# Kernel tuning notes

Hardware: AMD Instinct MI355X
Metric: run time of the kernel (lower is better)

Reference implementation:

```python
import jax, jax.numpy as jnp
import numpy as np

B, T, D_IN = 64, 1024, 12
H = 256          # hidden_dim
N_CLASSES = 17


def _lstm_dir(x, w_ih, w_hh, b_ih, b_hh, reverse):
    """Single-direction LSTM. x: [B,T,D]; w_ih: [4H,D]; w_hh: [4H,H]. Returns [B,T,H].
    Gate order follows PyTorch: i, f, g, o."""
    # Precompute input projection for all timesteps (big GEMM, compute-friendly)
    x_proj = jnp.einsum('btd,gd->btg', x, w_ih) + (b_ih + b_hh)  # [B,T,4H]
    x_proj = jnp.swapaxes(x_proj, 0, 1)  # [T,B,4H]
    h0 = jnp.zeros((x.shape[0], H), x.dtype)
    c0 = jnp.zeros((x.shape[0], H), x.dtype)

    def step(carry, xt):
        h, c = carry
        gates = xt + h @ w_hh.T  # [B,4H]
        i, f, g, o = jnp.split(gates, 4, axis=-1)
        c = jax.nn.sigmoid(f) * c + jax.nn.sigmoid(i) * jnp.tanh(g)
        h = jax.nn.sigmoid(o) * jnp.tanh(c)
        return (h, c), h

    _, hs = jax.lax.scan(step, (h0, c0), x_proj, reverse=reverse)  # hs: [T,B,H]
    return jnp.swapaxes(hs, 0, 1)  # [B,T,H]


def _bilstm_layer(x, w_ih, w_hh, b_ih, b_hh):
    """w_*: stacked [2, ...] for (forward, backward) directions."""
    fwd = _lstm_dir(x, w_ih[0], w_hh[0], b_ih[0], b_hh[0], reverse=False)
    bwd = _lstm_dir(x, w_ih[1], w_hh[1], b_ih[1], b_hh[1], reverse=True)
    return jnp.concatenate([fwd, bwd], axis=-1)  # [B,T,2H]


def setup_inputs() -> dict:
    key = jax.random.key(0)
    ks = jax.random.split(key, 11)
    s = 1.0 / np.sqrt(H)  # PyTorch LSTM init scale
    x = jax.random.normal(ks[0], (B, T, D_IN), dtype=jnp.float32)
    # Layer 0: input dim D_IN; Layer 1: input dim 2H (bidirectional outputs)
    w_ih0 = jax.random.uniform(ks[1], (2, 4 * H, D_IN), minval=-s, maxval=s)
    w_hh0 = jax.random.uniform(ks[2], (2, 4 * H, H), minval=-s, maxval=s)
    b_ih0 = jax.random.uniform(ks[3], (2, 4 * H), minval=-s, maxval=s)
    b_hh0 = jax.random.uniform(ks[4], (2, 4 * H), minval=-s, maxval=s)
    w_ih1 = jax.random.uniform(ks[5], (2, 4 * H, 2 * H), minval=-s, maxval=s)
    w_hh1 = jax.random.uniform(ks[6], (2, 4 * H, H), minval=-s, maxval=s)
    b_ih1 = jax.random.uniform(ks[7], (2, 4 * H), minval=-s, maxval=s)
    b_hh1 = jax.random.uniform(ks[8], (2, 4 * H), minval=-s, maxval=s)
    fc_w = jax.random.uniform(ks[9], (N_CLASSES, 2 * H), minval=-s, maxval=s)
    fc_b = jax.random.uniform(ks[10], (N_CLASSES,), minval=-s, maxval=s)
    return {"x": x, "w_ih0": w_ih0, "w_hh0": w_hh0, "b_ih0": b_ih0, "b_hh0": b_hh0,
            "w_ih1": w_ih1, "w_hh1": w_hh1, "b_ih1": b_ih1, "b_hh1": b_hh1,
            "fc_w": fc_w, "fc_b": fc_b}


def reference(x, w_ih0, w_hh0, b_ih0, b_hh0, w_ih1, w_hh1, b_ih1, b_hh1, fc_w, fc_b):
    # Eval mode: dropout layers are identity.
    h = _bilstm_layer(x, w_ih0, w_hh0, b_ih0, b_hh0)   # [B,T,2H]
    h = _bilstm_layer(h, w_ih1, w_hh1, b_ih1, b_hh1)   # [B,T,2H]
    pooled = h.mean(axis=1)                             # [B,2H]
    return pooled @ fc_w.T + fc_b                       # [B,n_classes]
```

## Files before the change

kernel.cpp:

```cpp
#include <hip/hip_runtime.h>

#define NB 64
#define NT 1024
#define DIN 12
#define NH 256
#define NG 1024
#define NCLS 17
#define TCL 128
#define NCHUNK 8
#define XPS ((size_t)2 * NB * TCL * NG)

typedef _Float16 f16;
typedef __attribute__((ext_vector_type(2))) _Float16 half2_t;
typedef __attribute__((ext_vector_type(8))) _Float16 f16x8;
typedef __attribute__((ext_vector_type(4))) float f32x4;
typedef unsigned int uint;
typedef unsigned short ushort;

__device__ __forceinline__ float sigm(float v) { return 1.0f / (1.0f + __expf(-v)); }
__device__ __forceinline__ float tanh_(float v) {
    v = fminf(fmaxf(v, -15.0f), 15.0f);
    float e = __expf(2.0f * v);
    return (e - 1.0f) / (e + 1.0f);
}
__device__ __forceinline__ float dot2(uint w, uint h, float c) {
    return __builtin_amdgcn_fdot2(__builtin_bit_cast(half2_t, w),
                                  __builtin_bit_cast(half2_t, h), c, false);
}
__device__ __forceinline__ uint pack16(float a, float b) {
    union { f16 h[2]; uint u; } cv; cv.h[0] = (f16)a; cv.h[1] = (f16)b; return cv.u;
}
__device__ __forceinline__ uint pkrtz(float a, float b) {
    return __builtin_bit_cast(uint, __builtin_amdgcn_cvt_pkrtz(a, b));
}
__device__ __forceinline__ ushort hbits(f16 v) {
    union { f16 h; ushort u; } cv; cv.h = v; return cv.u;
}

__global__ void k_prep(const float* __restrict__ w_hh0, const float* __restrict__ w_hh1,
                       const float* __restrict__ w_ih0, const float* __restrict__ w_ih1,
                       const float* __restrict__ b_ih1, const float* __restrict__ b_hh1,
                       uint* __restrict__ Wkv, uint* __restrict__ Wka,
                       uint* __restrict__ Wkl, uint* __restrict__ wih0p,
                       f16* __restrict__ wih1h, float* __restrict__ bsum1) {
    int i = blockIdx.x * 256 + threadIdx.x;
    if (i < 4 * 4 * 256 * 40) {
        int kp = i % 40; int r = i / 40;
        int t = r & 255, q = (r >> 8) & 3, ld = r >> 10;
        const float* row = (ld < 2 ? w_hh0 : w_hh1) + (size_t)(ld & 1) * NG * NH
                         + (size_t)(q * 256 + t) * NH;
        Wkv[i] = pack16(row[2 * kp], row[2 * kp + 1]);
    }
    if (i < 4 * 4 * 256 * 60) {
        int kp = 40 + (i % 60); int r = i / 60;
        int t = r & 255, q = (r >> 8) & 3, ld = r >> 10;
        const float* row = (ld < 2 ? w_hh0 : w_hh1) + (size_t)(ld & 1) * NG * NH
                         + (size_t)(q * 256 + t) * NH;
        Wka[i] = pack16(row[2 * kp], row[2 * kp + 1]);
    }
    if (i < 4 * 4 * 7 * 256 * 4) {
        int j = i & 3; int u = i >> 2;
        int t = u & 255; int v = u >> 8;
        int g = v % 7; int w2 = v / 7;
        int q = w2 & 3, ld = w2 >> 2;
        int kp = 100 + 4 * g + j;
        const float* row = (ld < 2 ? w_hh0 : w_hh1) + (size_t)(ld & 1) * NG * NH
                         + (size_t)(q * 256 + t) * NH;
        Wkl[i] = pack16(row[2 * kp], row[2 * kp + 1]);
    }
    if (i < 2 * 4 * 6 * 256) {
        int t = i & 255; int r = i >> 8;
        int dp = r % 6, q = (r / 6) & 3, dd = r / 24;
        const float* row = w_ih0 + ((size_t)dd * NG + q * 256 + t) * DIN;
        wih0p[i] = pack16(row[2 * dp], row[2 * dp + 1]);
    }
    if (i < 2 * NG * 2 * NH) wih1h[i] = (f16)w_ih1[i];
    if (i < 2 * NG) bsum1[i] = b_ih1[i] + b_hh1[i];
}

template <int LAYER>
__device__ void rec_seq(char* smem, int rb, int chunk, int nsteps,
                        const uint* __restrict__ Wkv, const uint* __restrict__ Wka,
                        const uint* __restrict__ Wkl, const uint* __restrict__ wih0p,
                        const float* __restrict__ b_ih0, const float* __restrict__ b_hh0,
                        const float* __restrict__ x, const float* __restrict__ xp1,
                        f16* __restrict__ out0h,
                        float* __restrict__ hst, float* __restrict__ cst,
                        float* __restrict__ hsm) {
    uint4* wlds4 = (uint4*)smem;
    ushort* hs16 = (ushort*)(smem + 114688);
    uint* wihl = (uint*)(smem + 115712);

    const int tid = threadIdx.x;
    const int dir = rb >> 6;
    const int b = rb & 63;
    const int ld = LAYER * 2 + dir;

    for (int n = tid; n < 7168; n += 256) wlds4[n] = ((const uint4*)Wkl)[ld * 7168 + n];
    if (LAYER == 0)
        for (int n = tid; n < 6144; n += 256) wihl[n] = wih0p[dir * 6144 + n];

    uint4 wrv[4][10];
    #pragma unroll
    for (int q = 0; q < 4; ++q) {
        const uint* src = Wkv + (size_t)((ld * 4 + q) * 256 + tid) * 40;
        #pragma unroll
        for (int m = 0; m < 10; ++m) wrv[q][m] = *(const uint4*)(src + m * 4);
    }

    uint aw[240];
    #pragma unroll
    for (int q = 0; q < 4; ++q) {
        const uint* src = Wka + (size_t)((ld * 4 + q) * 256 + tid) * 60;
        #pragma unroll
        for (int m = 0; m < 15; ++m) {
            uint4 v = *(const uint4*)(src + m * 4);
            asm volatile("v_accvgpr_write_b32 %0, %1" : "=a"(aw[(q * 15 + m) * 4 + 0]) : "v"(v.x));
            asm volatile("v_accvgpr_write_b32 %0, %1" : "=a"(aw[(q * 15 + m) * 4 + 1]) : "v"(v.y));
            asm volatile("v_accvgpr_write_b32 %0, %1" : "=a"(aw[(q * 15 + m) * 4 + 2]) : "v"(v.z));
            asm volatile("v_accvgpr_write_b32 %0, %1" : "=a"(aw[(q * 15 + m) * 4 + 3]) : "v"(v.w));
        }
    }

    float bias[4] = {0.f, 0.f, 0.f, 0.f};
    if (LAYER == 0) {
        #pragma unroll
        for (int q = 0; q < 4; ++q)
            bias[q] = b_ih0[dir * NG + q * 256 + tid] + b_hh0[dir * NG + q * 256 + tid];
    }

    const int sidx = (ld * NB + b) * NH + tid;
    float cv, hv, hsv = 0.f;
    if (chunk == 0) { cv = 0.f; hv = 0.f; }
    else {
        cv = cst[sidx]; hv = hst[sidx];
        if (LAYER == 1) hsv = hsm[(dir * NB + b) * NH + tid];
    }
    hs16[tid] = hbits((f16)hv);
    __syncthreads();

    #pragma unroll 1
    for (int it = 0; it < nsteps; ++it) {
        const int par = it & 1;
        const uint4* Hh = (const uint4*)(hs16 + par * 256);

        float ah[4] = {0, 0, 0, 0};

        float xv[12]; float4 xq4;
        if (LAYER == 0) {
            const int t = dir ? (NT - 1 - it) : it;
            const float4* xp = (const float4*)(x + ((size_t)b * NT + t) * DIN);
            float4 A = xp[0], B4 = xp[1], C4 = xp[2];
            xv[0] = A.x;  xv[1] = A.y;  xv[2] = A.z;  xv[3] = A.w;
            xv[4] = B4.x; xv[5] = B4.y; xv[6] = B4.z; xv[7] = B4.w;
            xv[8] = C4.x; xv[9] = C4.y; xv[10] = C4.z; xv[11] = C4.w;
        } else {
            xq4 = *(const float4*)(xp1 + (((size_t)dir * NB + b) * TCL + it) * NG + tid * 4);
        }

        #pragma unroll
        for (int g8 = 0; g8 < 10; ++g8) {
            uint4 Hhv = Hh[g8];
            #pragma unroll
            for (int q = 0; q < 4; ++q) {
                uint4 w = wrv[q][g8];
                ah[q] = dot2(w.x, Hhv.x, ah[q]);
                ah[q] = dot2(w.y, Hhv.y, ah[q]);
                ah[q] = dot2(w.z, Hhv.z, ah[q]);
                ah[q] = dot2(w.w, Hhv.w, ah[q]);
            }
        }
        #pragma unroll
        for (int m = 0; m < 15; ++m) {
            const int g8 = 10 + m;
            uint4 Hhv = Hh[g8];
            #pragma unroll
            for (int q = 0; q < 4; ++q) {
                uint w0, w1, w2, w3;
                asm volatile("v_accvgpr_read_b32 %0, %1" : "=v"(w0) : "a"(aw[(q * 15 + m) * 4 + 0]));
                asm volatile("v_accvgpr_read_b32 %0, %1" : "=v"(w1) : "a"(aw[(q * 15 + m) * 4 + 1]));
                asm volatile("v_accvgpr_read_b32 %0, %1" : "=v"(w2) : "a"(aw[(q * 15 + m) * 4 + 2]));
                asm volatile("v_accvgpr_read_b32 %0, %1" : "=v"(w3) : "a"(aw[(q * 15 + m) * 4 + 3]));
                ah[q] = dot2(w0, Hhv.x, ah[q]);
                ah[q] = dot2(w1, Hhv.y, ah[q]);
                ah[q] = dot2(w2, Hhv.z, ah[q]);
                ah[q] = dot2(w3, Hhv.w, ah[q]);
            }
        }
        #pragma unroll
        for (int g = 0; g < 7; ++g) {
            const int g8 = 25 + g;
            uint4 Hhv = Hh[g8];
            #pragma unroll
            for (int q = 0; q < 4; ++q) {
                uint4 w = wlds4[(q * 7 + g) * 256 + tid];
                ah[q] = dot2(w.x, Hhv.x, ah[q]);
                ah[q] = dot2(w.y, Hhv.y, ah[q]);
                ah[q] = dot2(w.z, Hhv.z, ah[q]);
                ah[q] = dot2(w.w, Hhv.w, ah[q]);
            }
        }

        float z[4];
        #pragma unroll
        for (int q = 0; q < 4; ++q) z[q] = ah[q];
        if (LAYER == 0) {
            uint xph[6];
            #pragma unroll
            for (int d = 0; d < 6; ++d) xph[d] = pkrtz(xv[2 * d], xv[2 * d + 1]);
            #pragma unroll
            for (int q = 0; q < 4; ++q) {
                float a = bias[q];
                #pragma unroll
                for (int d = 0; d < 6; ++d)
                    a = dot2(wihl[(q * 6 + d) * 256 + tid], xph[d], a);
                z[q] += a;
            }
        } else {
            z[0] += xq4.x; z[1] += xq4.y; z[2] += xq4.z; z[3] += xq4.w;
        }
        cv = sigm(z[1]) * cv + sigm(z[0]) * tanh_(z[2]);
        hv = sigm(z[3]) * tanh_(cv);
        if (LAYER == 1) hsv += hv;

        f16 hi = (f16)hv;
        hs16[(par ^ 1) * 256 + tid] = hbits(hi);
        if (LAYER == 0) {
            const int t = dir ? (NT - 1 - it) : it;
            out0h[((size_t)b * NT + t) * 512 + dir * 256 + tid] = hi;
        }
        __syncthreads();
    }

    cst[sidx] = cv; hst[sidx] = hv;
    if (LAYER == 1) hsm[(dir * NB + b) * NH + tid] = hsv;
}

__device__ void proj_role(int pb, int c,
                          const f16* __restrict__ out0h, const f16* __restrict__ wih1h,
                          const float* __restrict__ bsum1, float* __restrict__ xp1) {
    const int tid = threadIdx.x;
    const int w = tid >> 6, l = tid & 63;
    const int lane16 = l & 15, quad = l >> 4;

    #pragma unroll 1
    for (int mi = 0; mi < 2; ++mi) {
        const int mtg = pb * 8 + w * 2 + mi;
        const int dirt = mtg >> 9;
        const int mtl = mtg & 511;

        const int ra = mtl * 16 + lane16;
        const int ab = ra >> 7, tla = ra & 127;
        const int ta = dirt ? (NT - 1 - c * TCL - tla) : (c * TCL + tla);
        const f16* Arow = out0h + ((size_t)ab * NT + ta) * 512 + quad * 8;

        uint4 afr[16];
        #pragma unroll
        for (int kt = 0; kt < 16; ++kt) afr[kt] = *(const uint4*)(Arow + kt * 32);

        int ob[4], otl[4];
        #pragma unroll
        for (int reg = 0; reg < 4; ++reg) {
            int rr = mtl * 16 + quad * 4 + reg;
            ob[reg] = rr >> 7; otl[reg] = rr & 127;
        }

        const f16* Bbase = wih1h + (size_t)dirt * NG * 512 + quad * 8;

        #pragma unroll 1
        for (int nt = 0; nt < 64; ++nt) {
            const int col = nt * 16 + lane16;
            const f16* Brow = Bbase + (size_t)col * 512;
            float bias = bsum1[dirt * NG + col];

            f32x4 acc = {0.f, 0.f, 0.f, 0.f};
            #pragma unroll
            for (int kt = 0; kt < 16; ++kt) {
                uint4 bv = *(const uint4*)(Brow + kt * 32);
                acc = __builtin_amdgcn_mfma_f32_16x16x32_f16(
                    __builtin_bit_cast(f16x8, afr[kt]),
                    __builtin_bit_cast(f16x8, bv), acc, 0, 0, 0);
            }
            const int ucol = col & 255, qcol = col >> 8;
            #pragma unroll
            for (int reg = 0; reg < 4; ++reg) {
                xp1[((size_t)(dirt * NB + ob[reg]) * TCL + otl[reg]) * NG
                    + ucol * 4 + qcol] = acc[reg] + bias;
            }
        }
    }
}

__global__ __launch_bounds__(256, 1) void k_rec0(
    const uint* __restrict__ Wkv, const uint* __restrict__ Wka,
    const uint* __restrict__ Wkl, const uint* __restrict__ wih0p,
    const float* __restrict__ b_ih0, const float* __restrict__ b_hh0,
    const float* __restrict__ x, f16* __restrict__ out0h,
    float* __restrict__ hst, float* __restrict__ cst) {
    extern __shared__ __align__(16) char smem[];
    rec_seq<0>(smem, blockIdx.x, 0, NT, Wkv, Wka, Wkl, wih0p, b_ih0, b_hh0,
               x, nullptr, out0h, hst, cst, nullptr);
}

__global__ __launch_bounds__(256, 1) void k_pipe(
    int j,
    const uint* __restrict__ Wkv, const uint* __restrict__ Wka,
    const uint* __restrict__ Wkl,
    const f16* __restrict__ out0h, const f16* __restrict__ wih1h,
    const float* __restrict__ bsum1, float* __restrict__ xp1,
    float* __restrict__ hst, float* __restrict__ cst, float* __restrict__ hsm) {
    extern __shared__ __align__(16) char smem[];
    const int bid = blockIdx.x;
    if (bid < 128) {
        const int cc = j - 1;
        if (cc >= 0 && cc < NCHUNK)
            rec_seq<1>(smem, bid, cc, TCL, Wkv, Wka, Wkl, nullptr, nullptr, nullptr,
                       nullptr, xp1 + (size_t)(cc & 1) * XPS, nullptr, hst, cst, hsm);
    } else {
        const int cp = j;
        if (cp < NCHUNK)
            proj_role(bid - 128, cp, out0h, wih1h, bsum1,
                      xp1 + (size_t)(cp & 1) * XPS);
    }
}

__global__ void k_fc(const float* __restrict__ hsm, const float* __restrict__ fc_w,
                     const float* __restrict__ fc_b, float* __restrict__ out) {
    const int b = blockIdx.x;
    const int n = threadIdx.x;
    if (n >= NCLS) return;
    float acc = fc_b[n];
    const float inv = 1.0f / (float)NT;
    for (int k = 0; k < 2 * NH; ++k) {
        float pv = hsm[((k >> 8) * NB + b) * NH + (k & 255)];
        acc += (pv * inv) * fc_w[n * 2 * NH + k];
    }
    out[b * NCLS + n] = acc;
}

extern "C" void kernel_launch(void* const* d_in, const int* in_sizes, int n_in,
                              void* d_out, int out_size, void* d_ws, size_t ws_size,
                              hipStream_t stream) {
    const float* x     = (const float*)d_in[0];
    const float* w_ih0 = (const float*)d_in[1];
    const float* w_hh0 = (const float*)d_in[2];
    const float* b_ih0 = (const float*)d_in[3];
    const float* b_hh0 = (const float*)d_in[4];
    const float* w_ih1 = (const float*)d_in[5];
    const float* w_hh1 = (const float*)d_in[6];
    const float* b_ih1 = (const float*)d_in[7];
    const float* b_hh1 = (const float*)d_in[8];
    const float* fc_w  = (const float*)d_in[9];
    const float* fc_b  = (const float*)d_in[10];
    float* out = (float*)d_out;

    char* ws = (char*)d_ws;
    uint* Wkv   = (uint*)ws;
    uint* Wka   = Wkv + 163840;
    uint* Wkl   = Wka + 245760;
    uint* wih0p = Wkl + 114688;
    f16* wih1h  = (f16*)(wih0p + 12288);
    float* bsum1 = (float*)(wih1h + 1048576);
    float* hst  = bsum1 + 2048;
    float* cst  = hst + 65536;
    float* hsm  = cst + 65536;
    float* xp1  = hsm + 32768;
    f16* out0h  = (f16*)(xp1 + 2 * XPS);

    k_prep<<<dim3(4096), dim3(256), 0, stream>>>(
        w_hh0, w_hh1, w_ih0, w_ih1, b_ih1, b_hh1,
        Wkv, Wka, Wkl, wih0p, wih1h, bsum1);

    k_rec0<<<dim3(128), dim3(256), 140288, stream>>>(
        Wkv, Wka, Wkl, wih0p, b_ih0, b_hh0, x, out0h, hst, cst);

    for (int j = 0; j <= NCHUNK; ++j) {
        k_pipe<<<dim3(256), dim3(256), 115712, stream>>>(
            j, Wkv, Wka, Wkl, out0h, wih1h, bsum1, xp1, hst, cst, hsm);
    }

    k_fc<<<dim3(64), dim3(32), 0, stream>>>(hsm, fc_w, fc_b, out);
}
```

Measured before the change: 4.978 ms.

## Split LSTM recurrence K-dimension across two thread halves per block

Each recurrent block now runs 512 threads. Each hidden unit's 256-wide dot product is split into two K halves, one per thread group, and the partial gate sums are combined through shared memory with an extra barrier per step. Weight packing is reorganised so each half keeps a smaller set of weights in VGPRs/AGPRs and the remainder in LDS. The projection role now handles one M tile per wave, since twice as many waves are available. This shortens the serial per-step dot-product chain at the cost of an additional __syncthreads and LDS exchange on every timestep.

```diff
diff --git a/kernel.cpp b/kernel.cpp
--- a/kernel.cpp
+++ b/kernel.cpp
@@ -44,35 +44,37 @@
                        uint* __restrict__ Wkl, uint* __restrict__ wih0p,
                        f16* __restrict__ wih1h, float* __restrict__ bsum1) {
     int i = blockIdx.x * 256 + threadIdx.x;
-    if (i < 4 * 4 * 256 * 40) {
-        int kp = i % 40; int r = i / 40;
-        int t = r & 255, q = (r >> 8) & 3, ld = r >> 10;
+    if (i < 131072) {
+        int kpi = i & 15; int r = i >> 4;
+        int u = r & 255, pp = (r >> 8) & 1, q = (r >> 9) & 3, ld = r >> 11;
         const float* row = (ld < 2 ? w_hh0 : w_hh1) + (size_t)(ld & 1) * NG * NH
-                         + (size_t)(q * 256 + t) * NH;
+                         + (size_t)(q * 256 + u) * NH;
+        int kp = 64 * pp + kpi;
         Wkv[i] = pack16(row[2 * kp], row[2 * kp + 1]);
     }
-    if (i < 4 * 4 * 256 * 60) {
-        int kp = 40 + (i % 60); int r = i / 60;
-        int t = r & 255, q = (r >> 8) & 3, ld = r >> 10;
+    if (i < 262144) {
+        int kpi = i & 31; int r = i >> 5;
+        int u = r & 255, pp = (r >> 8) & 1, q = (r >> 9) & 3, ld = r >> 11;
         const float* row = (ld < 2 ? w_hh0 : w_hh1) + (size_t)(ld & 1) * NG * NH
-                         + (size_t)(q * 256 + t) * NH;
+                         + (size_t)(q * 256 + u) * NH;
+        int kp = 64 * pp + 16 + kpi;
         Wka[i] = pack16(row[2 * kp], row[2 * kp + 1]);
     }
-    if (i < 4 * 4 * 7 * 256 * 4) {
-        int j = i & 3; int u = i >> 2;
-        int t = u & 255; int v = u >> 8;
-        int g = v % 7; int w2 = v / 7;
-        int q = w2 & 3, ld = w2 >> 2;
-        int kp = 100 + 4 * g + j;
+    if (i < 131072) {
+        int j = i & 3; int r4 = i >> 2;
+        int u = r4 & 255, pp = (r4 >> 8) & 1, g4 = (r4 >> 9) & 3;
+        int q = (r4 >> 11) & 3, ld = r4 >> 13;
         const float* row = (ld < 2 ? w_hh0 : w_hh1) + (size_t)(ld & 1) * NG * NH
-                         + (size_t)(q * 256 + t) * NH;
+                         + (size_t)(q * 256 + u) * NH;
+        int kp = 64 * pp + 48 + 4 * g4 + j;
         Wkl[i] = pack16(row[2 * kp], row[2 * kp + 1]);
     }
-    if (i < 2 * 4 * 6 * 256) {
-        int t = i & 255; int r = i >> 8;
-        int dp = r % 6, q = (r / 6) & 3, dd = r / 24;
-        const float* row = w_ih0 + ((size_t)dd * NG + q * 256 + t) * DIN;
-        wih0p[i] = pack16(row[2 * dp], row[2 * dp + 1]);
+    if (i < 12288) {
+        int dp = i % 3; int r = i / 3;
+        int u = r & 255, pp = (r >> 8) & 1, q = (r >> 9) & 3, dd = r >> 11;
+        const float* row = w_ih0 + ((size_t)dd * NG + q * 256 + u) * DIN;
+        int d0 = 6 * pp + 2 * dp;
+        wih0p[i] = pack16(row[d0], row[d0 + 1]);
     }
     if (i < 2 * NG * 2 * NH) wih1h[i] = (f16)w_ih1[i];
     if (i < 2 * NG) bsum1[i] = b_ih1[i] + b_hh1[i];
@@ -81,159 +83,166 @@
 template <int LAYER>
 __device__ void rec_seq(char* smem, int rb, int chunk, int nsteps,
                         const uint* __restrict__ Wkv, const uint* __restrict__ Wka,
-                        const uint* __restrict__ Wkl, const uint* __restrict__ wih0p,
+                        const uint4* __restrict__ Wkl, const uint* __restrict__ wih0p,
                         const float* __restrict__ b_ih0, const float* __restrict__ b_hh0,
                         const float* __restrict__ x, const float* __restrict__ xp1,
                         f16* __restrict__ out0h,
                         float* __restrict__ hst, float* __restrict__ cst,
                         float* __restrict__ hsm) {
     uint4* wlds4 = (uint4*)smem;
-    ushort* hs16 = (ushort*)(smem + 114688);
-    uint* wihl = (uint*)(smem + 115712);
-
+    float* zx = (float*)(smem + 131072);
+    ushort* hs16 = (ushort*)(smem + 135168);
     const int tid = threadIdx.x;
-    const int dir = rb >> 6;
-    const int b = rb & 63;
+    const int u = tid & 255, p = tid >> 8;
+    const int dir = rb >> 6, b = rb & 63;
     const int ld = LAYER * 2 + dir;
 
-    for (int n = tid; n < 7168; n += 256) wlds4[n] = ((const uint4*)Wkl)[ld * 7168 + n];
-    if (LAYER == 0)
-        for (int n = tid; n < 6144; n += 256) wihl[n] = wih0p[dir * 6144 + n];
-
-    uint4 wrv[4][10];
+    for (int n = tid; n < 8192; n += 512) wlds4[n] = Wkl[ld * 8192 + n];
+
+    uint4 wrv[4][4];
     #pragma unroll
     for (int q = 0; q < 4; ++q) {
-        const uint* src = Wkv + (size_t)((ld * 4 + q) * 256 + tid) * 40;
-        #pragma unroll
-        for (int m = 0; m < 10; ++m) wrv[q][m] = *(const uint4*)(src + m * 4);
-    }
-
-    uint aw[240];
+        const uint* src = Wkv + (size_t)((((ld * 4 + q) * 2 + p) * 256) + u) * 16;
+        #pragma unroll
+        for (int gi = 0; gi < 4; ++gi) wrv[q][gi] = *(const uint4*)(src + gi * 4);
+    }
+    uint aw[128];
     #pragma unroll
     for (int q = 0; q < 4; ++q) {
-        const uint* src = Wka + (size_t)((ld * 4 + q) * 256 + tid) * 60;
-        #pragma unroll
-        for (int m = 0; m < 15; ++m) {
-            uint4 v = *(const uint4*)(src + m * 4);
-            asm volatile("v_accvgpr_write_b32 %0, %1" : "=a"(aw[(q * 15 + m) * 4 + 0]) : "v"(v.x));
-            asm volatile("v_accvgpr_write_b32 %0, %1" : "=a"(aw[(q * 15 + m) * 4 + 1]) : "v"(v.y));
-            asm volatile("v_accvgpr_write_b32 %0, %1" : "=a"(aw[(q * 15 + m) * 4 + 2]) : "v"(v.z));
-            asm volatile("v_accvgpr_write_b32 %0, %1" : "=a"(aw[(q * 15 + m) * 4 + 3]) : "v"(v.w));
-        }
-    }
-
+        const uint* src = Wka + (size_t)((((ld * 4 + q) * 2 + p) * 256) + u) * 32;
+        #pragma unroll
+        for (int ga = 0; ga < 8; ++ga) {
+            uint4 v = *(const uint4*)(src + ga * 4);
+            asm volatile("v_accvgpr_write_b32 %0, %1" : "=a"(aw[(q * 8 + ga) * 4 + 0]) : "v"(v.x));
+            asm volatile("v_accvgpr_write_b32 %0, %1" : "=a"(aw[(q * 8 + ga) * 4 + 1]) : "v"(v.y));
+            asm volatile("v_accvgpr_write_b32 %0, %1" : "=a"(aw[(q * 8 + ga) * 4 + 2]) : "v"(v.z));
+            asm volatile("v_accvgpr_write_b32 %0, %1" : "=a"(aw[(q * 8 + ga) * 4 + 3]) : "v"(v.w));
+        }
+    }
+
+    uint wihr[12];
+    if (LAYER == 0) {
+        #pragma unroll
+        for (int q = 0; q < 4; ++q) {
+            const uint* src = wih0p + (size_t)((((dir * 4 + q) * 2 + p) * 256) + u) * 3;
+            wihr[q * 3 + 0] = src[0]; wihr[q * 3 + 1] = src[1]; wihr[q * 3 + 2] = src[2];
+        }
+    }
     float bias[4] = {0.f, 0.f, 0.f, 0.f};
-    if (LAYER == 0) {
+    if (LAYER == 0 && p == 0) {
         #pragma unroll
         for (int q = 0; q < 4; ++q)
-            bias[q] = b_ih0[dir * NG + q * 256 + tid] + b_hh0[dir * NG + q * 256 + tid];
-    }
-
-    const int sidx = (ld * NB + b) * NH + tid;
-    float cv, hv, hsv = 0.f;
-    if (chunk == 0) { cv = 0.f; hv = 0.f; }
-    else {
-        cv = cst[sidx]; hv = hst[sidx];
-        if (LAYER == 1) hsv = hsm[(dir * NB + b) * NH + tid];
-    }
-    hs16[tid] = hbits((f16)hv);
+            bias[q] = b_ih0[dir * NG + q * 256 + u] + b_hh0[dir * NG + q * 256 + u];
+    }
+
+    const int sidx = (ld * NB + b) * NH + u;
+    float cv = 0.f, hv = 0.f, hsv = 0.f;
+    if (p == 0) {
+        if (chunk != 0) {
+            cv = cst[sidx]; hv = hst[sidx];
+            if (LAYER == 1) hsv = hsm[(dir * NB + b) * NH + u];
+        }
+        hs16[u] = hbits((f16)hv);
+    }
     __syncthreads();
 
     #pragma unroll 1
     for (int it = 0; it < nsteps; ++it) {
-        const int par = it & 1;
-        const uint4* Hh = (const uint4*)(hs16 + par * 256);
-
-        float ah[4] = {0, 0, 0, 0};
-
-        float xv[12]; float4 xq4;
-        if (LAYER == 0) {
+        const uint4* Hh = ((const uint4*)hs16) + 16 * p;
+
+        float4 xq4 = {0.f, 0.f, 0.f, 0.f};
+        float xvp[6];
+        if (LAYER == 1) {
+            if (p == 0)
+                xq4 = *(const float4*)(xp1 + (((size_t)dir * NB + b) * TCL + it) * NG + u * 4);
+        } else {
             const int t = dir ? (NT - 1 - it) : it;
             const float4* xp = (const float4*)(x + ((size_t)b * NT + t) * DIN);
             float4 A = xp[0], B4 = xp[1], C4 = xp[2];
-            xv[0] = A.x;  xv[1] = A.y;  xv[2] = A.z;  xv[3] = A.w;
-            xv[4] = B4.x; xv[5] = B4.y; xv[6] = B4.z; xv[7] = B4.w;
-            xv[8] = C4.x; xv[9] = C4.y; xv[10] = C4.z; xv[11] = C4.w;
-        } else {
-            xq4 = *(const float4*)(xp1 + (((size_t)dir * NB + b) * TCL + it) * NG + tid * 4);
-        }
-
-        #pragma unroll
-        for (int g8 = 0; g8 < 10; ++g8) {
-            uint4 Hhv = Hh[g8];
+            if (p == 0) { xvp[0]=A.x; xvp[1]=A.y; xvp[2]=A.z; xvp[3]=A.w; xvp[4]=B4.x; xvp[5]=B4.y; }
+            else        { xvp[0]=B4.z; xvp[1]=B4.w; xvp[2]=C4.x; xvp[3]=C4.y; xvp[4]=C4.z; xvp[5]=C4.w; }
+        }
+
+        float ah[4] = {0.f, 0.f, 0.f, 0.f};
+
+        #pragma unroll
+        for (int gi = 0; gi < 4; ++gi) {
+            uint4 H = Hh[gi];
             #pragma unroll
             for (int q = 0; q < 4; ++q) {
-                uint4 w = wrv[q][g8];
-                ah[q] = dot2(w.x, Hhv.x, ah[q]);
-                ah[q] = dot2(w.y, Hhv.y, ah[q]);
-                ah[q] = dot2(w.z, Hhv.z, ah[q]);
-                ah[q] = dot2(w.w, Hhv.w, ah[q]);
-            }
-        }
-        #pragma unroll
-        for (int m = 0; m < 15; ++m) {
-            const int g8 = 10 + m;
-            uint4 Hhv = Hh[g8];
+                uint4 w = wrv[q][gi];
+                ah[q] = dot2(w.x, H.x, ah[q]);
+                ah[q] = dot2(w.y, H.y, ah[q]);
+                ah[q] = dot2(w.z, H.z, ah[q]);
+                ah[q] = dot2(w.w, H.w, ah[q]);
+            }
+        }
+        #pragma unroll
+        for (int ga = 0; ga < 8; ++ga) {
+            uint4 H = Hh[4 + ga];
             #pragma unroll
             for (int q = 0; q < 4; ++q) {
                 uint w0, w1, w2, w3;
-                asm volatile("v_accvgpr_read_b32 %0, %1" : "=v"(w0) : "a"(aw[(q * 15 + m) * 4 + 0]));
-                asm volatile("v_accvgpr_read_b32 %0, %1" : "=v"(w1) : "a"(aw[(q * 15 + m) * 4 + 1]));
-                asm volatile("v_accvgpr_read_b32 %0, %1" : "=v"(w2) : "a"(aw[(q * 15 + m) * 4 + 2]));
-                asm volatile("v_accvgpr_read_b32 %0, %1" : "=v"(w3) : "a"(aw[(q * 15 + m) * 4 + 3]));
-                ah[q] = dot2(w0, Hhv.x, ah[q]);
-                ah[q] = dot2(w1, Hhv.y, ah[q]);
-                ah[q] = dot2(w2, Hhv.z, ah[q]);
-                ah[q] = dot2(w3, Hhv.w, ah[q]);
-            }
-        }
-        #pragma unroll
-        for (int g = 0; g < 7; ++g) {
-            const int g8 = 25 + g;
-            uint4 Hhv = Hh[g8];
+                asm volatile("v_accvgpr_read_b32 %0, %1" : "=v"(w0) : "a"(aw[(q * 8 + ga) * 4 + 0]));
+                asm volatile("v_accvgpr_read_b32 %0, %1" : "=v"(w1) : "a"(aw[(q * 8 + ga) * 4 + 1]));
+                asm volatile("v_accvgpr_read_b32 %0, %1" : "=v"(w2) : "a"(aw[(q * 8 + ga) * 4 + 2]));
+                asm volatile("v_accvgpr_read_b32 %0, %1" : "=v"(w3) : "a"(aw[(q * 8 + ga) * 4 + 3]));
+                ah[q] = dot2(w0, H.x, ah[q]);
+                ah[q] = dot2(w1, H.y, ah[q]);
+                ah[q] = dot2(w2, H.z, ah[q]);
+                ah[q] = dot2(w3, H.w, ah[q]);
+            }
+        }
+        #pragma unroll
+        for (int g4 = 0; g4 < 4; ++g4) {
+            uint4 H = Hh[12 + g4];
             #pragma unroll
             for (int q = 0; q < 4; ++q) {
-                uint4 w = wlds4[(q * 7 + g) * 256 + tid];
-                ah[q] = dot2(w.x, Hhv.x, ah[q]);
-                ah[q] = dot2(w.y, Hhv.y, ah[q]);
-                ah[q] = dot2(w.z, Hhv.z, ah[q]);
-                ah[q] = dot2(w.w, Hhv.w, ah[q]);
-            }
-        }
-
-        float z[4];
-        #pragma unroll
-        for (int q = 0; q < 4; ++q) z[q] = ah[q];
+                uint4 w = wlds4[((q * 4 + g4) * 2 + p) * 256 + u];
+                ah[q] = dot2(w.x, H.x, ah[q]);
+                ah[q] = dot2(w.y, H.y, ah[q]);
+                ah[q] = dot2(w.z, H.z, ah[q]);
+                ah[q] = dot2(w.w, H.w, ah[q]);
+            }
+        }
         if (LAYER == 0) {
-            uint xph[6];
-            #pragma unroll
-            for (int d = 0; d < 6; ++d) xph[d] = pkrtz(xv[2 * d], xv[2 * d + 1]);
+            uint xph[3];
+            #pragma unroll
+            for (int dp = 0; dp < 3; ++dp) xph[dp] = pkrtz(xvp[2 * dp], xvp[2 * dp + 1]);
             #pragma unroll
             for (int q = 0; q < 4; ++q) {
-                float a = bias[q];
-                #pragma unroll
-                for (int d = 0; d < 6; ++d)
-                    a = dot2(wihl[(q * 6 + d) * 256 + tid], xph[d], a);
-                z[q] += a;
-            }
-        } else {
-            z[0] += xq4.x; z[1] += xq4.y; z[2] += xq4.z; z[3] += xq4.w;
-        }
-        cv = sigm(z[1]) * cv + sigm(z[0]) * tanh_(z[2]);
-        hv = sigm(z[3]) * tanh_(cv);
-        if (LAYER == 1) hsv += hv;
-
-        f16 hi = (f16)hv;
-        hs16[(par ^ 1) * 256 + tid] = hbits(hi);
-        if (LAYER == 0) {
-            const int t = dir ? (NT - 1 - it) : it;
-            out0h[((size_t)b * NT + t) * 512 + dir * 256 + tid] = hi;
-        }
+                ah[q] = dot2(wihr[q * 3 + 0], xph[0], ah[q]);
+                ah[q] = dot2(wihr[q * 3 + 1], xph[1], ah[q]);
+                ah[q] = dot2(wihr[q * 3 + 2], xph[2], ah[q]);
+            }
+        }
+
+        if (p == 1) *(float4*)(zx + u * 4) = make_float4(ah[0], ah[1], ah[2], ah[3]);
         __syncthreads();
-    }
-
-    cst[sidx] = cv; hst[sidx] = hv;
-    if (LAYER == 1) hsm[(dir * NB + b) * NH + tid] = hsv;
+
+        if (p == 0) {
+            float4 zo = *(const float4*)(zx + u * 4);
+            float z0 = ah[0] + zo.x + bias[0] + xq4.x;
+            float z1 = ah[1] + zo.y + bias[1] + xq4.y;
+            float z2 = ah[2] + zo.z + bias[2] + xq4.z;
+            float z3 = ah[3] + zo.w + bias[3] + xq4.w;
+            cv = sigm(z1) * cv + sigm(z0) * tanh_(z2);
+            hv = sigm(z3) * tanh_(cv);
+            if (LAYER == 1) hsv += hv;
+            f16 hi = (f16)hv;
+            hs16[u] = hbits(hi);
+            if (LAYER == 0) {
+                const int t = dir ? (NT - 1 - it) : it;
+                out0h[((size_t)b * NT + t) * 512 + dir * 256 + u] = hi;
+            }
+        }
+        __syncthreads();
+    }
+
+    if (p == 0) {
+        cst[sidx] = cv; hst[sidx] = hv;
+        if (LAYER == 1) hsm[(dir * NB + b) * NH + u] = hsv;
+    }
 }
 
 __device__ void proj_role(int pb, int c,
@@ -242,58 +251,54 @@
     const int tid = threadIdx.x;
     const int w = tid >> 6, l = tid & 63;
     const int lane16 = l & 15, quad = l >> 4;
+    const int mtg = pb * 8 + w;
+    const int dirt = mtg >> 9;
+    const int mtl = mtg & 511;
+
+    const int ra = mtl * 16 + lane16;
+    const int ab = ra >> 7, tla = ra & 127;
+    const int ta = dirt ? (NT - 1 - c * TCL - tla) : (c * TCL + tla);
+    const f16* Arow = out0h + ((size_t)ab * NT + ta) * 512 + quad * 8;
+
+    uint4 afr[16];
+    #pragma unroll
+    for (int kt = 0; kt < 16; ++kt) afr[kt] = *(const uint4*)(Arow + kt * 32);
+
+    int ob[4], otl[4];
+    #pragma unroll
+    for (int reg = 0; reg < 4; ++reg) {
+        int rr = mtl * 16 + quad * 4 + reg;
+        ob[reg] = rr >> 7; otl[reg] = rr & 127;
+    }
+
+    const f16* Bbase = wih1h + (size_t)dirt * NG * 512 + quad * 8;
 
     #pragma unroll 1
-    for (int mi = 0; mi < 2; ++mi) {
-        const int mtg = pb * 8 + w * 2 + mi;
-        const int dirt = mtg >> 9;
-        const int mtl = mtg & 511;
-
-        const int ra = mtl * 16 + lane16;
-        const int ab = ra >> 7, tla = ra & 127;
-        const int ta = dirt ? (NT - 1 - c * TCL - tla) : (c * TCL + tla);
-        const f16* Arow = out0h + ((size_t)ab * NT + ta) * 512 + quad * 8;
-
-        uint4 afr[16];
-        #pragma unroll
-        for (int kt = 0; kt < 16; ++kt) afr[kt] = *(const uint4*)(Arow + kt * 32);
-
-        int ob[4], otl[4];
+    for (int nt = 0; nt < 64; ++nt) {
+        const int col = nt * 16 + lane16;
+        const f16* Brow = Bbase + (size_t)col * 512;
+        float bias = bsum1[dirt * NG + col];
+
+        f32x4 acc = {0.f, 0.f, 0.f, 0.f};
+        #pragma unroll
+        for (int kt = 0; kt < 16; ++kt) {
+            uint4 bv = *(const uint4*)(Brow + kt * 32);
+            acc = __builtin_amdgcn_mfma_f32_16x16x32_f16(
+                __builtin_bit_cast(f16x8, afr[kt]),
+                __builtin_bit_cast(f16x8, bv), acc, 0, 0, 0);
+        }
+        const int ucol = col & 255, qcol = col >> 8;
         #pragma unroll
         for (int reg = 0; reg < 4; ++reg) {
-            int rr = mtl * 16 + quad * 4 + reg;
-            ob[reg] = rr >> 7; otl[reg] = rr & 127;
-        }
-
-        const f16* Bbase = wih1h + (size_t)dirt * NG * 512 + quad * 8;
-
-        #pragma unroll 1
-        for (int nt = 0; nt < 64; ++nt) {
-            const int col = nt * 16 + lane16;
-            const f16* Brow = Bbase + (size_t)col * 512;
-            float bias = bsum1[dirt * NG + col];
-
-            f32x4 acc = {0.f, 0.f, 0.f, 0.f};
-            #pragma unroll
-            for (int kt = 0; kt < 16; ++kt) {
-                uint4 bv = *(const uint4*)(Brow + kt * 32);
-                acc = __builtin_amdgcn_mfma_f32_16x16x32_f16(
-                    __builtin_bit_cast(f16x8, afr[kt]),
-                    __builtin_bit_cast(f16x8, bv), acc, 0, 0, 0);
-            }
-            const int ucol = col & 255, qcol = col >> 8;
-            #pragma unroll
-            for (int reg = 0; reg < 4; ++reg) {
-                xp1[((size_t)(dirt * NB + ob[reg]) * TCL + otl[reg]) * NG
-                    + ucol * 4 + qcol] = acc[reg] + bias;
-            }
-        }
-    }
-}
-
-__global__ __launch_bounds__(256, 1) void k_rec0(
+            xp1[((size_t)(dirt * NB + ob[reg]) * TCL + otl[reg]) * NG
+                + ucol * 4 + qcol] = acc[reg] + bias;
+        }
+    }
+}
+
+__global__ __launch_bounds__(512) void k_rec0(
     const uint* __restrict__ Wkv, const uint* __restrict__ Wka,
-    const uint* __restrict__ Wkl, const uint* __restrict__ wih0p,
+    const uint4* __restrict__ Wkl, const uint* __restrict__ wih0p,
     const float* __restrict__ b_ih0, const float* __restrict__ b_hh0,
     const float* __restrict__ x, f16* __restrict__ out0h,
     float* __restrict__ hst, float* __restrict__ cst) {
@@ -302,10 +307,10 @@
                x, nullptr, out0h, hst, cst, nullptr);
 }
 
-__global__ __launch_bounds__(256, 1) void k_pipe(
+__global__ __launch_bounds__(512) void k_pipe(
     int j,
     const uint* __restrict__ Wkv, const uint* __restrict__ Wka,
-    const uint* __restrict__ Wkl,
+    const uint4* __restrict__ Wkl,
     const f16* __restrict__ out0h, const f16* __restrict__ wih1h,
     const float* __restrict__ bsum1, float* __restrict__ xp1,
     float* __restrict__ hst, float* __restrict__ cst, float* __restrict__ hsm) {
@@ -356,9 +361,9 @@
 
     char* ws = (char*)d_ws;
     uint* Wkv   = (uint*)ws;
-    uint* Wka   = Wkv + 163840;
-    uint* Wkl   = Wka + 245760;
-    uint* wih0p = Wkl + 114688;
+    uint* Wka   = Wkv + 131072;
+    uint* Wkl   = Wka + 262144;
+    uint* wih0p = Wkl + 131072;
     f16* wih1h  = (f16*)(wih0p + 12288);
     float* bsum1 = (float*)(wih1h + 1048576);
     float* hst  = bsum1 + 2048;
@@ -371,12 +376,12 @@
         w_hh0, w_hh1, w_ih0, w_ih1, b_ih1, b_hh1,
         Wkv, Wka, Wkl, wih0p, wih1h, bsum1);
 
-    k_rec0<<<dim3(128), dim3(256), 140288, stream>>>(
-        Wkv, Wka, Wkl, wih0p, b_ih0, b_hh0, x, out0h, hst, cst);
+    k_rec0<<<dim3(128), dim3(512), 135680, stream>>>(
+        Wkv, Wka, (const uint4*)Wkl, wih0p, b_ih0, b_hh0, x, out0h, hst, cst);
 
     for (int j = 0; j <= NCHUNK; ++j) {
-        k_pipe<<<dim3(256), dim3(256), 115712, stream>>>(
-            j, Wkv, Wka, Wkl, out0h, wih1h, bsum1, xp1, hst, cst, hsm);
+        k_pipe<<<dim3(256), dim3(512), 135680, stream>>>(
+            j, Wkv, Wka, (const uint4*)Wkl, out0h, wih1h, bsum1, xp1, hst, cst, hsm);
     }
 
     k_fc<<<dim3(64), dim3(32), 0, stream>>>(hsm, fc_w, fc_b, out);
```

Result: slower. 5.232 ms (+5.1%).
